# Performance work log

Measured on AMD Instinct MI355X. Metric: run time of the kernel, lower is better.

## Reference

```python
import jax, jax.numpy as jnp
import numpy as np

NEG_SLOPE = 0.2

def leaky_relu(x):
    return jnp.where(x >= 0, x, NEG_SLOPE * x)

def conv1x1(x, w, b):
    # x: [n,c,h,w], w: [o,c], b: [o]
    return jnp.einsum('nchw,oc->nohw', x, w) + b[None, :, None, None]

def setup_inputs() -> dict:
    key = jax.random.key(0)
    ks = jax.random.split(key, 7)
    n, c, h, w = 4, 64, 80, 80
    scale = 1.0 / np.sqrt(c)
    return {
        'x': jax.random.normal(ks[0], (n, c, h, w), dtype=jnp.float32),
        'w1': jax.random.normal(ks[1], (c, c), dtype=jnp.float32) * scale,
        'b1': jax.random.normal(ks[2], (c,), dtype=jnp.float32) * 0.01,
        'w2': jax.random.normal(ks[3], (c, c), dtype=jnp.float32) * scale,
        'b2': jax.random.normal(ks[4], (c,), dtype=jnp.float32) * 0.01,
        'w3': jax.random.normal(ks[5], (c, c), dtype=jnp.float32) * scale,
        'b3': jax.random.normal(ks[6], (c,), dtype=jnp.float32) * 0.01,
    }

def reference(x, w1, b1, w2, b2, w3, b3):
    n, c, h, w = x.shape
    e1 = leaky_relu(conv1x1(x, w1, b1))  # [n,c,h,w]
    e2 = leaky_relu(conv1x1(x, w2, b2))
    asm = leaky_relu(conv1x1(x, w3, b3))
    # q: [n, hw, c]; k: [n, c, hw]
    q = e1.transpose(0, 2, 3, 1).reshape(n, h * w, c)
    k = e2.reshape(n, c, h * w)
    score = jax.nn.softmax(jnp.matmul(q, k), axis=2)  # [n, hw, hw]
    v = asm.reshape(n, c, h * w).transpose(0, 2, 1)   # [n, hw, c]
    out = jnp.matmul(score, v)                        # [n, hw, c]
    return out.transpose(0, 2, 1).reshape(n, c, h, w)
```

## Files before the change

### kernel.cpp

```cpp
#include <hip/hip_runtime.h>


typedef __attribute__((ext_vector_type(8))) unsigned short us8;
typedef __attribute__((ext_vector_type(4))) unsigned short us4;
typedef __attribute__((ext_vector_type(8))) __bf16 bf16x8;
typedef __attribute__((ext_vector_type(16))) float f32x16;

#define HW 6400
#define L2E 1.44269504088896340736f
#define SHIFT 32.0f
#define KS 10
#define ITERS 10

union V8 { us8 s; us4 h[2]; bf16x8 b; unsigned u4[4]; };

__device__ __forceinline__ unsigned short f32_to_bf16(float f) {
  unsigned u = __float_as_uint(f);
  u += 0x7fffu + ((u >> 16) & 1u);
  return (unsigned short)(u >> 16);
}
__device__ __forceinline__ float bf16_bits_to_f32(unsigned short u) {
  return __uint_as_float(((unsigned)u) << 16);
}
__device__ __forceinline__ unsigned pack_bf16x2(float a, float b) {
#if __has_builtin(__builtin_amdgcn_cvt_pk_bf16_f32)
  auto v = __builtin_amdgcn_cvt_pk_bf16_f32(a, b);
  unsigned u;
  __builtin_memcpy(&u, &v, 4);
  return u;
#else
  unsigned ua = __float_as_uint(a); ua += 0x7fffu + ((ua >> 16) & 1u);
  unsigned ub = __float_as_uint(b); ub += 0x7fffu + ((ub >> 16) & 1u);
  return (ua >> 16) | (ub & 0xffff0000u);
#endif
}

__device__ __forceinline__ void split_hilo(const float* f, V8& hi, V8& lo) {
#pragma unroll
  for (int j = 0; j < 8; ++j) {
    const unsigned short h = f32_to_bf16(f[j]);
    const float r = f[j] - bf16_bits_to_f32(h);
    hi.s[j] = h;
    lo.s[j] = f32_to_bf16(r);
  }
}

__global__ __launch_bounds__(256, 2) void conv_kernel(
    const float* __restrict__ x,
    const float* __restrict__ w1, const float* __restrict__ b1,
    const float* __restrict__ w2, const float* __restrict__ b2,
    const float* __restrict__ w3, const float* __restrict__ b3,
    unsigned short* __restrict__ Qg, unsigned short* __restrict__ Kg,
    unsigned short* __restrict__ Vg) {
  __shared__ __align__(16) float xs[64 * 132];
  __shared__ __align__(16) unsigned short tb[128 * 72];

  const int t = threadIdx.x;
  const int n = blockIdx.y;
  const int p0 = blockIdx.x * 128;
  const int wv = t >> 6;
  const int lane = t & 63;
  const int l31 = lane & 31;
  const int lh = lane >> 5;
  const int ob = (wv & 1) * 32;
  const int pw = (wv >> 1) * 64;

  {
    const int c = t >> 2, qq = t & 3;
    const float* src = x + ((size_t)(n * 64 + c) * HW + p0 + qq * 32);
    float* dst = xs + c * 132 + qq * 32;
#pragma unroll
    for (int i = 0; i < 8; ++i)
      *(float4*)(dst + i * 4) = *(const float4*)(src + i * 4);
  }
  __syncthreads();

  const float* wms[3] = {w1, w2, w3};
  const float* bms[3] = {b1, b2, b3};

#pragma unroll 1
  for (int k = 0; k < 3; ++k) {
    const float* wm = wms[k];
    const float* bm = bms[k];

    V8 ah[4], al[4];
#pragma unroll
    for (int kst = 0; kst < 4; ++kst) {
      const float* wr = wm + (size_t)(ob + l31) * 64 + kst * 16 + lh * 8;
      float wf[8];
      *(float4*)(wf) = *(const float4*)wr;
      *(float4*)(wf + 4) = *(const float4*)(wr + 4);
      split_hilo(wf, ah[kst], al[kst]);
    }

    f32x16 acc[2];
#pragma unroll
    for (int pb = 0; pb < 2; ++pb)
#pragma unroll
      for (int r = 0; r < 16; ++r) acc[pb][r] = 0.f;

#pragma unroll
    for (int kst = 0; kst < 4; ++kst) {
#pragma unroll
      for (int pb = 0; pb < 2; ++pb) {
        float xf[8];
        const float* xp = xs + (kst * 16 + lh * 8) * 132 + pw + pb * 32 + l31;
#pragma unroll
        for (int j = 0; j < 8; ++j) xf[j] = xp[j * 132];
        V8 bh, bl;
        split_hilo(xf, bh, bl);
        acc[pb] = __builtin_amdgcn_mfma_f32_32x32x16_bf16(al[kst].b, bh.b, acc[pb], 0, 0, 0);
        acc[pb] = __builtin_amdgcn_mfma_f32_32x32x16_bf16(ah[kst].b, bl.b, acc[pb], 0, 0, 0);
        acc[pb] = __builtin_amdgcn_mfma_f32_32x32x16_bf16(ah[kst].b, bh.b, acc[pb], 0, 0, 0);
      }
    }

    if (k < 2) {
#pragma unroll
      for (int pb = 0; pb < 2; ++pb) {
#pragma unroll
        for (int rq = 0; rq < 4; ++rq) {
          const int o = ob + 8 * rq + 4 * lh;
          const int pcol = pw + pb * 32 + l31;
          float v[4];
#pragma unroll
          for (int j = 0; j < 4; ++j) {
            float a = acc[pb][4 * rq + j] + bm[o + j];
            a = fmaxf(a, 0.f) + 0.2f * fminf(a, 0.f);
            if (k == 0) a *= L2E;
            v[j] = a;
          }
          unsigned* dst = (unsigned*)(tb + pcol * 72 + o);
          dst[0] = pack_bf16x2(v[0], v[1]);
          dst[1] = pack_bf16x2(v[2], v[3]);
        }
      }
      __syncthreads();
      {
        const int p = t >> 1, half = t & 1;
        const unsigned short* src = tb + p * 72 + half * 32;
        unsigned short* dst = (k == 0 ? Qg : Kg) +
                              (size_t)(n * HW + p0 + p) * 64 + half * 32;
#pragma unroll
        for (int i = 0; i < 4; ++i) *(us8*)(dst + i * 8) = *(const us8*)(src + i * 8);
      }
      __syncthreads();
    } else {
#pragma unroll
      for (int pb = 0; pb < 2; ++pb) {
#pragma unroll
        for (int r = 0; r < 16; ++r) {
          const int o = ob + 8 * (r >> 2) + 4 * lh + (r & 3);
          const int pcol = pw + pb * 32 + l31;
          float a = acc[pb][r] + bm[o];
          a = fmaxf(a, 0.f) + 0.2f * fminf(a, 0.f);
          Vg[(size_t)(n * 64 + o) * HW + p0 + pcol] = f32_to_bf16(a);
        }
      }
    }
  }
}

__global__ __launch_bounds__(256, 2) void attn_kernel(
    const unsigned short* __restrict__ Qg, const unsigned short* __restrict__ Kg,
    const unsigned short* __restrict__ Vg, unsigned short* __restrict__ Opart,
    float* __restrict__ Lpart) {
  __shared__ __align__(16) char smem[36864];
  unsigned short* Otb = (unsigned short*)smem;

  const int t = threadIdx.x;
  const int w = t >> 6;
  const int lane = t & 63;
  const int l31 = lane & 31;
  const int lh = lane >> 5;
  const int nb = blockIdx.y;
  const int qb = blockIdx.x * 256;
  const int ks = blockIdx.z;
  const int key0 = ks * (HW / KS);

  V8 aQ[2][4];
#pragma unroll
  for (int qh = 0; qh < 2; ++qh) {
    const unsigned short* qrow =
        Qg + (size_t)(nb * HW + qb + w * 64 + qh * 32 + l31) * 64 + lh * 8;
#pragma unroll
    for (int kst = 0; kst < 4; ++kst) aQ[qh][kst].s = *(const us8*)(qrow + kst * 16);
  }

  f32x16 accO[2][2];
#pragma unroll
  for (int qh = 0; qh < 2; ++qh)
#pragma unroll
    for (int ci = 0; ci < 2; ++ci)
#pragma unroll
      for (int r = 0; r < 16; ++r) accO[qh][ci][r] = 0.f;
  float lp[2] = {0.f, 0.f};

  const int soff = (t >> 2) * 72 + (t & 3) * 16;
  const unsigned short* ksrc =
      Kg + (size_t)nb * HW * 64 + (size_t)(key0 + (t >> 2)) * 64 + (t & 3) * 16;
  const unsigned short* vsrc =
      Vg + (size_t)nb * 64 * HW + (size_t)(t >> 2) * HW + key0 + (t & 3) * 16;

  V8 kr0, kr1, vr0, vr1;
  kr0.s = *(const us8*)ksrc;
  kr1.s = *(const us8*)(ksrc + 8);
  vr0.s = *(const us8*)vsrc;
  vr1.s = *(const us8*)(vsrc + 8);
  {
    unsigned short* kd = (unsigned short*)smem + soff;
    unsigned short* vd = (unsigned short*)(smem + 18432) + soff;
    *(us8*)kd = kr0.s; *(us8*)(kd + 8) = kr1.s;
    *(us8*)vd = vr0.s; *(us8*)(vd + 8) = vr1.s;
  }
  __syncthreads();

#pragma unroll 1
  for (int jt = 0; jt < ITERS; ++jt) {
    const int b = jt & 1;
    const unsigned short* Kc = (const unsigned short*)(smem + b * 9216);
    const unsigned short* Vc = (const unsigned short*)(smem + 18432 + b * 9216);
    const bool more = (jt + 1 < ITERS);

    if (more) {
      kr0.s = *(const us8*)(ksrc + (jt + 1) * 4096);
      kr1.s = *(const us8*)(ksrc + (jt + 1) * 4096 + 8);
      vr0.s = *(const us8*)(vsrc + (jt + 1) * 64);
      vr1.s = *(const us8*)(vsrc + (jt + 1) * 64 + 8);
    }

    V8 ak[2][4];
#pragma unroll
    for (int ni = 0; ni < 2; ++ni)
#pragma unroll
      for (int kst = 0; kst < 4; ++kst)
        ak[ni][kst].s = *(const us8*)(Kc + (ni * 32 + l31) * 72 + kst * 16 + lh * 8);

    uint2 pkq[2][2][4];
#pragma unroll
    for (int qh = 0; qh < 2; ++qh) {
#pragma unroll
      for (int ni = 0; ni < 2; ++ni) {
        f32x16 sacc;
#pragma unroll
        for (int r = 0; r < 16; ++r) sacc[r] = -SHIFT;
#pragma unroll
        for (int kst = 0; kst < 4; ++kst)
          sacc = __builtin_amdgcn_mfma_f32_32x32x16_bf16(ak[ni][kst].b,
                                                         aQ[qh][kst].b, sacc, 0, 0, 0);
#pragma unroll
        for (int g = 0; g < 4; ++g) {
          const float p0 = __builtin_amdgcn_exp2f(sacc[4 * g + 0]);
          const float p1 = __builtin_amdgcn_exp2f(sacc[4 * g + 1]);
          const float p2 = __builtin_amdgcn_exp2f(sacc[4 * g + 2]);
          const float p3 = __builtin_amdgcn_exp2f(sacc[4 * g + 3]);
          lp[qh] += (p0 + p1) + (p2 + p3);
          pkq[qh][ni][g].x = pack_bf16x2(p0, p1);
          pkq[qh][ni][g].y = pack_bf16x2(p2, p3);
        }
      }
    }

    V8 bv[2][4];
#pragma unroll
    for (int ci = 0; ci < 2; ++ci)
#pragma unroll
      for (int kst = 0; kst < 4; ++kst)
        bv[ci][kst].s = *(const us8*)(Vc + (ci * 32 + l31) * 72 + kst * 16 + lh * 8);

#pragma unroll
    for (int qh = 0; qh < 2; ++qh) {
#pragma unroll
      for (int kst = 0; kst < 4; ++kst) {
        const int ni = kst >> 1;
        const int gb = 2 * (kst & 1);
        const uint2 qa = pkq[qh][ni][gb];
        const uint2 qb2 = pkq[qh][ni][gb + 1];
        uint2 send;
        send.x = lh ? qa.x : qb2.x;
        send.y = lh ? qa.y : qb2.y;
        uint2 recv;
        recv.x = __shfl_xor(send.x, 32);
        recv.y = __shfl_xor(send.y, 32);
        const uint2 keep = {lh ? qb2.x : qa.x, lh ? qb2.y : qa.y};
        V8 ap;
        ap.u4[0] = lh ? recv.x : keep.x;
        ap.u4[1] = lh ? recv.y : keep.y;
        ap.u4[2] = lh ? keep.x : recv.x;
        ap.u4[3] = lh ? keep.y : recv.y;
        accO[qh][0] = __builtin_amdgcn_mfma_f32_32x32x16_bf16(ap.b, bv[0][kst].b,
                                                              accO[qh][0], 0, 0, 0);
        accO[qh][1] = __builtin_amdgcn_mfma_f32_32x32x16_bf16(ap.b, bv[1][kst].b,
                                                              accO[qh][1], 0, 0, 0);
      }
    }

    if (more) {
      unsigned short* kd = (unsigned short*)(smem + (1 - b) * 9216) + soff;
      unsigned short* vd = (unsigned short*)(smem + 18432 + (1 - b) * 9216) + soff;
      *(us8*)kd = kr0.s; *(us8*)(kd + 8) = kr1.s;
      *(us8*)vd = vr0.s; *(us8*)(vd + 8) = vr1.s;
      __syncthreads();
    }
  }

#pragma unroll
  for (int qh = 0; qh < 2; ++qh) {
    const float lsum = lp[qh] + __shfl_xor(lp[qh], 32);
    if (lh == 0)
      Lpart[((size_t)ks * 4 + nb) * HW + qb + w * 64 + qh * 32 + l31] = lsum;
  }

#pragma unroll 1
  for (int pi = 0; pi < 2; ++pi) {
    __syncthreads();
    if ((w >> 1) == pi) {
#pragma unroll
      for (int qh = 0; qh < 2; ++qh)
#pragma unroll
        for (int ci = 0; ci < 2; ++ci)
#pragma unroll
          for (int r = 0; r < 16; ++r) {
            const int qcol = (w & 1) * 64 + qh * 32 + 8 * (r >> 2) + 4 * lh + (r & 3);
            Otb[(ci * 32 + l31) * 132 + qcol] = f32_to_bf16(accO[qh][ci][r]);
          }
    }
    __syncthreads();
    {
      const int ch = t >> 2, part = t & 3;
      const unsigned short* src = Otb + ch * 132 + part * 32;
      unsigned short* dst = Opart + (((size_t)ks * 4 + nb) * 64 + ch) * HW +
                            qb + pi * 128 + part * 32;
#pragma unroll
      for (int i = 0; i < 4; ++i) {
        V8 v;
        v.h[0] = *(const us4*)(src + i * 8);
        v.h[1] = *(const us4*)(src + i * 8 + 4);
        *(us8*)(dst + i * 8) = v.s;
      }
    }
  }
}

__global__ __launch_bounds__(256) void combine_kernel(
    const unsigned short* __restrict__ Opart, const float* __restrict__ Lpart,
    float* __restrict__ out) {
  const int tid = blockIdx.x * 256 + threadIdx.x;
  const size_t e = (size_t)tid * 4;
  float4 o = {0.f, 0.f, 0.f, 0.f};
#pragma unroll
  for (int ks = 0; ks < KS; ++ks) {
    const us4 v = *(const us4*)(Opart + (size_t)ks * (4 * 64 * HW) + e);
    o.x += bf16_bits_to_f32(v[0]);
    o.y += bf16_bits_to_f32(v[1]);
    o.z += bf16_bits_to_f32(v[2]);
    o.w += bf16_bits_to_f32(v[3]);
  }
  const int n = (int)(e / (64 * HW));
  const int p = (int)(e % HW);
  float4 l = {0.f, 0.f, 0.f, 0.f};
#pragma unroll
  for (int ks = 0; ks < KS; ++ks) {
    const float4 v = *(const float4*)(Lpart + ((size_t)ks * 4 + n) * HW + p);
    l.x += v.x; l.y += v.y; l.z += v.z; l.w += v.w;
  }
  float4 r;
  r.x = o.x / l.x; r.y = o.y / l.y; r.z = o.z / l.z; r.w = o.w / l.w;
  *(float4*)(out + e) = r;
}

extern "C" void kernel_launch(void* const* d_in, const int* in_sizes, int n_in,
                              void* d_out, int out_size, void* d_ws, size_t ws_size,
                              hipStream_t stream) {
  const float* x = (const float*)d_in[0];
  const float* w1 = (const float*)d_in[1];
  const float* b1 = (const float*)d_in[2];
  const float* w2 = (const float*)d_in[3];
  const float* b2 = (const float*)d_in[4];
  const float* w3 = (const float*)d_in[5];
  const float* b3 = (const float*)d_in[6];
  float* out = (float*)d_out;

  unsigned short* Q = (unsigned short*)d_ws;
  unsigned short* K = Q + (size_t)4 * HW * 64;
  unsigned short* V = K + (size_t)4 * HW * 64;
  unsigned short* Opart = V + (size_t)4 * HW * 64;
  float* Lpart = (float*)(Opart + (size_t)KS * 4 * 64 * HW);

  conv_kernel<<<dim3(50, 4), 256, 0, stream>>>(x, w1, b1, w2, b2, w3, b3,
                                               Q, K, V);
  attn_kernel<<<dim3(25, 4, KS), 256, 0, stream>>>(Q, K, V, Opart, Lpart);
  combine_kernel<<<1600, 256, 0, stream>>>(Opart, Lpart, out);
}
```

Baseline: 155.5 us.

## Load attention K/V fragments directly from global memory, drop LDS staging

The attention kernel stops staging K and V tiles through double-buffered shared memory with per-iteration barriers. Each wave now reads its MFMA operand fragments straight from global memory (relying on L1/L2 for reuse across the four waves). The loop is reorganized per key-half so S, softmax exp and PV run in smaller chunks with fewer live registers. Occupancy hint rises to 3 blocks per CU, and the grid is flattened to a 1D launch with a remapped block index that places blocks sharing the same batch and key split close together for cache locality. Risks are redundant global/L2 traffic (each wave fetches the same K/V) and exposed load latency without software prefetch.

```diff
diff --git a/kernel.cpp b/kernel.cpp
--- a/kernel.cpp
+++ b/kernel.cpp
@@ -161,21 +161,24 @@
   }
 }
 
-__global__ __launch_bounds__(256, 2) void attn_kernel(
+__global__ __launch_bounds__(256, 3) void attn_kernel(
     const unsigned short* __restrict__ Qg, const unsigned short* __restrict__ Kg,
     const unsigned short* __restrict__ Vg, unsigned short* __restrict__ Opart,
     float* __restrict__ Lpart) {
-  __shared__ __align__(16) char smem[36864];
-  unsigned short* Otb = (unsigned short*)smem;
+  __shared__ __align__(16) unsigned short Otb[64 * 132];
 
   const int t = threadIdx.x;
   const int w = t >> 6;
   const int lane = t & 63;
   const int l31 = lane & 31;
   const int lh = lane >> 5;
-  const int nb = blockIdx.y;
-  const int qb = blockIdx.x * 256;
-  const int ks = blockIdx.z;
+
+  const int id = blockIdx.x;
+  const int nb = (id >> 1) & 3;
+  const int j = ((id >> 3) << 1) | (id & 1);
+  const int qi = j % 25;
+  const int ks = j / 25;
+  const int qb = qi * 256;
   const int key0 = ks * (HW / KS);
 
   V8 aQ[2][4];
@@ -196,58 +199,40 @@
       for (int r = 0; r < 16; ++r) accO[qh][ci][r] = 0.f;
   float lp[2] = {0.f, 0.f};
 
-  const int soff = (t >> 2) * 72 + (t & 3) * 16;
-  const unsigned short* ksrc =
-      Kg + (size_t)nb * HW * 64 + (size_t)(key0 + (t >> 2)) * 64 + (t & 3) * 16;
-  const unsigned short* vsrc =
-      Vg + (size_t)nb * 64 * HW + (size_t)(t >> 2) * HW + key0 + (t & 3) * 16;
-
-  V8 kr0, kr1, vr0, vr1;
-  kr0.s = *(const us8*)ksrc;
-  kr1.s = *(const us8*)(ksrc + 8);
-  vr0.s = *(const us8*)vsrc;
-  vr1.s = *(const us8*)(vsrc + 8);
-  {
-    unsigned short* kd = (unsigned short*)smem + soff;
-    unsigned short* vd = (unsigned short*)(smem + 18432) + soff;
-    *(us8*)kd = kr0.s; *(us8*)(kd + 8) = kr1.s;
-    *(us8*)vd = vr0.s; *(us8*)(vd + 8) = vr1.s;
-  }
-  __syncthreads();
+  const unsigned short* kfrag =
+      Kg + (size_t)(nb * HW + key0 + l31) * 64 + lh * 8;
+  const unsigned short* vfrag =
+      Vg + (size_t)nb * 64 * HW + (size_t)l31 * HW + key0 + lh * 8;
 
 #pragma unroll 1
   for (int jt = 0; jt < ITERS; ++jt) {
-    const int b = jt & 1;
-    const unsigned short* Kc = (const unsigned short*)(smem + b * 9216);
-    const unsigned short* Vc = (const unsigned short*)(smem + 18432 + b * 9216);
-    const bool more = (jt + 1 < ITERS);
-
-    if (more) {
-      kr0.s = *(const us8*)(ksrc + (jt + 1) * 4096);
-      kr1.s = *(const us8*)(ksrc + (jt + 1) * 4096 + 8);
-      vr0.s = *(const us8*)(vsrc + (jt + 1) * 64);
-      vr1.s = *(const us8*)(vsrc + (jt + 1) * 64 + 8);
-    }
-
-    V8 ak[2][4];
-#pragma unroll
-    for (int ni = 0; ni < 2; ++ni)
+    const unsigned short* kit = kfrag + jt * 4096;
+    const unsigned short* vit = vfrag + jt * 64;
+
+#pragma unroll
+    for (int ni = 0; ni < 2; ++ni) {
+      V8 ak[4];
 #pragma unroll
       for (int kst = 0; kst < 4; ++kst)
-        ak[ni][kst].s = *(const us8*)(Kc + (ni * 32 + l31) * 72 + kst * 16 + lh * 8);
-
-    uint2 pkq[2][2][4];
-#pragma unroll
-    for (int qh = 0; qh < 2; ++qh) {
-#pragma unroll
-      for (int ni = 0; ni < 2; ++ni) {
+        ak[kst].s = *(const us8*)(kit + ni * 2048 + kst * 16);
+      V8 bv[2][2];
+#pragma unroll
+      for (int ci = 0; ci < 2; ++ci)
+#pragma unroll
+        for (int kk = 0; kk < 2; ++kk)
+          bv[ci][kk].s =
+              *(const us8*)(vit + (size_t)ci * 32 * HW + (2 * ni + kk) * 16);
+
+#pragma unroll
+      for (int qh = 0; qh < 2; ++qh) {
         f32x16 sacc;
 #pragma unroll
         for (int r = 0; r < 16; ++r) sacc[r] = -SHIFT;
 #pragma unroll
         for (int kst = 0; kst < 4; ++kst)
-          sacc = __builtin_amdgcn_mfma_f32_32x32x16_bf16(ak[ni][kst].b,
+          sacc = __builtin_amdgcn_mfma_f32_32x32x16_bf16(ak[kst].b,
                                                          aQ[qh][kst].b, sacc, 0, 0, 0);
+        uint2 pkg[4];
 #pragma unroll
         for (int g = 0; g < 4; ++g) {
           const float p0 = __builtin_amdgcn_exp2f(sacc[4 * g + 0]);
@@ -255,52 +240,32 @@
           const float p2 = __builtin_amdgcn_exp2f(sacc[4 * g + 2]);
           const float p3 = __builtin_amdgcn_exp2f(sacc[4 * g + 3]);
           lp[qh] += (p0 + p1) + (p2 + p3);
-          pkq[qh][ni][g].x = pack_bf16x2(p0, p1);
-          pkq[qh][ni][g].y = pack_bf16x2(p2, p3);
+          pkg[g].x = pack_bf16x2(p0, p1);
+          pkg[g].y = pack_bf16x2(p2, p3);
         }
-      }
-    }
-
-    V8 bv[2][4];
-#pragma unroll
-    for (int ci = 0; ci < 2; ++ci)
-#pragma unroll
-      for (int kst = 0; kst < 4; ++kst)
-        bv[ci][kst].s = *(const us8*)(Vc + (ci * 32 + l31) * 72 + kst * 16 + lh * 8);
-
-#pragma unroll
-    for (int qh = 0; qh < 2; ++qh) {
-#pragma unroll
-      for (int kst = 0; kst < 4; ++kst) {
-        const int ni = kst >> 1;
-        const int gb = 2 * (kst & 1);
-        const uint2 qa = pkq[qh][ni][gb];
-        const uint2 qb2 = pkq[qh][ni][gb + 1];
-        uint2 send;
-        send.x = lh ? qa.x : qb2.x;
-        send.y = lh ? qa.y : qb2.y;
-        uint2 recv;
-        recv.x = __shfl_xor(send.x, 32);
-        recv.y = __shfl_xor(send.y, 32);
-        const uint2 keep = {lh ? qb2.x : qa.x, lh ? qb2.y : qa.y};
-        V8 ap;
-        ap.u4[0] = lh ? recv.x : keep.x;
-        ap.u4[1] = lh ? recv.y : keep.y;
-        ap.u4[2] = lh ? keep.x : recv.x;
-        ap.u4[3] = lh ? keep.y : recv.y;
-        accO[qh][0] = __builtin_amdgcn_mfma_f32_32x32x16_bf16(ap.b, bv[0][kst].b,
-                                                              accO[qh][0], 0, 0, 0);
-        accO[qh][1] = __builtin_amdgcn_mfma_f32_32x32x16_bf16(ap.b, bv[1][kst].b,
-                                                              accO[qh][1], 0, 0, 0);
-      }
-    }
-
-    if (more) {
-      unsigned short* kd = (unsigned short*)(smem + (1 - b) * 9216) + soff;
-      unsigned short* vd = (unsigned short*)(smem + 18432 + (1 - b) * 9216) + soff;
-      *(us8*)kd = kr0.s; *(us8*)(kd + 8) = kr1.s;
-      *(us8*)vd = vr0.s; *(us8*)(vd + 8) = vr1.s;
-      __syncthreads();
+#pragma unroll
+        for (int kk = 0; kk < 2; ++kk) {
+          const int gb = 2 * kk;
+          const uint2 qa = pkg[gb];
+          const uint2 qb2 = pkg[gb + 1];
+          uint2 send;
+          send.x = lh ? qa.x : qb2.x;
+          send.y = lh ? qa.y : qb2.y;
+          uint2 recv;
+          recv.x = __shfl_xor(send.x, 32);
+          recv.y = __shfl_xor(send.y, 32);
+          const uint2 keep = {lh ? qb2.x : qa.x, lh ? qb2.y : qa.y};
+          V8 ap;
+          ap.u4[0] = lh ? recv.x : keep.x;
+          ap.u4[1] = lh ? recv.y : keep.y;
+          ap.u4[2] = lh ? keep.x : recv.x;
+          ap.u4[3] = lh ? keep.y : recv.y;
+          accO[qh][0] = __builtin_amdgcn_mfma_f32_32x32x16_bf16(
+              ap.b, bv[0][kk].b, accO[qh][0], 0, 0, 0);
+          accO[qh][1] = __builtin_amdgcn_mfma_f32_32x32x16_bf16(
+              ap.b, bv[1][kk].b, accO[qh][1], 0, 0, 0);
+        }
+      }
     }
   }
 
@@ -389,6 +354,6 @@
 
   conv_kernel<<<dim3(50, 4), 256, 0, stream>>>(x, w1, b1, w2, b2, w3, b3,
                                                Q, K, V);
-  attn_kernel<<<dim3(25, 4, KS), 256, 0, stream>>>(Q, K, V, Opart, Lpart);
+  attn_kernel<<<1000, 256, 0, stream>>>(Q, K, V, Opart, Lpart);
   combine_kernel<<<1600, 256, 0, stream>>>(Opart, Lpart, out);
 }
```

Result: slower. 346.0 us (+122.6%).

## Shrink per-wave query tile and halve key splits to raise attention occupancy

Applied to the files above, without the earlier changes.

Each wave now handles 32 queries instead of 64, so a block covers 128 queries. The split-K factor drops from 10 to 5, with twice as many key iterations per block, and launch bounds allow 4 blocks per CU. The smaller register footprint is meant to raise occupancy, and fewer key splits reduce the partial-output traffic written and then read by the combine kernel. In exchange, each K/V tile in shared memory is reused across fewer queries, which doubles LDS reads per flop. The constant score shift of -32 is removed, which relies on the scores staying within exp2 range.

```diff
diff --git a/kernel.cpp b/kernel.cpp
--- a/kernel.cpp
+++ b/kernel.cpp
@@ -8,9 +8,8 @@
 
 #define HW 6400
 #define L2E 1.44269504088896340736f
-#define SHIFT 32.0f
-#define KS 10
-#define ITERS 10
+#define KS 5
+#define ITERS 20
 
 union V8 { us8 s; us4 h[2]; bf16x8 b; unsigned u4[4]; };
 
@@ -161,7 +160,7 @@
   }
 }
 
-__global__ __launch_bounds__(256, 2) void attn_kernel(
+__global__ __launch_bounds__(256, 4) void attn_kernel(
     const unsigned short* __restrict__ Qg, const unsigned short* __restrict__ Kg,
     const unsigned short* __restrict__ Vg, unsigned short* __restrict__ Opart,
     float* __restrict__ Lpart) {
@@ -174,27 +173,24 @@
   const int l31 = lane & 31;
   const int lh = lane >> 5;
   const int nb = blockIdx.y;
-  const int qb = blockIdx.x * 256;
+  const int qb = blockIdx.x * 128;
   const int ks = blockIdx.z;
   const int key0 = ks * (HW / KS);
 
-  V8 aQ[2][4];
-#pragma unroll
-  for (int qh = 0; qh < 2; ++qh) {
+  V8 aQ[4];
+  {
     const unsigned short* qrow =
-        Qg + (size_t)(nb * HW + qb + w * 64 + qh * 32 + l31) * 64 + lh * 8;
-#pragma unroll
-    for (int kst = 0; kst < 4; ++kst) aQ[qh][kst].s = *(const us8*)(qrow + kst * 16);
-  }
-
-  f32x16 accO[2][2];
-#pragma unroll
-  for (int qh = 0; qh < 2; ++qh)
-#pragma unroll
-    for (int ci = 0; ci < 2; ++ci)
-#pragma unroll
-      for (int r = 0; r < 16; ++r) accO[qh][ci][r] = 0.f;
-  float lp[2] = {0.f, 0.f};
+        Qg + (size_t)(nb * HW + qb + w * 32 + l31) * 64 + lh * 8;
+#pragma unroll
+    for (int kst = 0; kst < 4; ++kst) aQ[kst].s = *(const us8*)(qrow + kst * 16);
+  }
+
+  f32x16 accO[2];
+#pragma unroll
+  for (int ci = 0; ci < 2; ++ci)
+#pragma unroll
+    for (int r = 0; r < 16; ++r) accO[ci][r] = 0.f;
+  float lp = 0.f;
 
   const int soff = (t >> 2) * 72 + (t & 3) * 16;
   const unsigned short* ksrc =
@@ -229,53 +225,43 @@
       vr1.s = *(const us8*)(vsrc + (jt + 1) * 64 + 8);
     }
 
-    V8 ak[2][4];
-#pragma unroll
-    for (int ni = 0; ni < 2; ++ni)
+#pragma unroll
+    for (int ni = 0; ni < 2; ++ni) {
+      V8 ak[4];
 #pragma unroll
       for (int kst = 0; kst < 4; ++kst)
-        ak[ni][kst].s = *(const us8*)(Kc + (ni * 32 + l31) * 72 + kst * 16 + lh * 8);
-
-    uint2 pkq[2][2][4];
-#pragma unroll
-    for (int qh = 0; qh < 2; ++qh) {
-#pragma unroll
-      for (int ni = 0; ni < 2; ++ni) {
-        f32x16 sacc;
-#pragma unroll
-        for (int r = 0; r < 16; ++r) sacc[r] = -SHIFT;
-#pragma unroll
-        for (int kst = 0; kst < 4; ++kst)
-          sacc = __builtin_amdgcn_mfma_f32_32x32x16_bf16(ak[ni][kst].b,
-                                                         aQ[qh][kst].b, sacc, 0, 0, 0);
-#pragma unroll
-        for (int g = 0; g < 4; ++g) {
-          const float p0 = __builtin_amdgcn_exp2f(sacc[4 * g + 0]);
-          const float p1 = __builtin_amdgcn_exp2f(sacc[4 * g + 1]);
-          const float p2 = __builtin_amdgcn_exp2f(sacc[4 * g + 2]);
-          const float p3 = __builtin_amdgcn_exp2f(sacc[4 * g + 3]);
-          lp[qh] += (p0 + p1) + (p2 + p3);
-          pkq[qh][ni][g].x = pack_bf16x2(p0, p1);
-          pkq[qh][ni][g].y = pack_bf16x2(p2, p3);
-        }
-      }
-    }
-
-    V8 bv[2][4];
-#pragma unroll
-    for (int ci = 0; ci < 2; ++ci)
+        ak[kst].s = *(const us8*)(Kc + (ni * 32 + l31) * 72 + kst * 16 + lh * 8);
+      f32x16 sacc;
+#pragma unroll
+      for (int r = 0; r < 16; ++r) sacc[r] = 0.f;
 #pragma unroll
       for (int kst = 0; kst < 4; ++kst)
-        bv[ci][kst].s = *(const us8*)(Vc + (ci * 32 + l31) * 72 + kst * 16 + lh * 8);
-
-#pragma unroll
-    for (int qh = 0; qh < 2; ++qh) {
-#pragma unroll
-      for (int kst = 0; kst < 4; ++kst) {
-        const int ni = kst >> 1;
-        const int gb = 2 * (kst & 1);
-        const uint2 qa = pkq[qh][ni][gb];
-        const uint2 qb2 = pkq[qh][ni][gb + 1];
+        sacc = __builtin_amdgcn_mfma_f32_32x32x16_bf16(ak[kst].b, aQ[kst].b,
+                                                       sacc, 0, 0, 0);
+      uint2 pkg[4];
+#pragma unroll
+      for (int g = 0; g < 4; ++g) {
+        const float p0 = __builtin_amdgcn_exp2f(sacc[4 * g + 0]);
+        const float p1 = __builtin_amdgcn_exp2f(sacc[4 * g + 1]);
+        const float p2 = __builtin_amdgcn_exp2f(sacc[4 * g + 2]);
+        const float p3 = __builtin_amdgcn_exp2f(sacc[4 * g + 3]);
+        lp += (p0 + p1) + (p2 + p3);
+        pkg[g].x = pack_bf16x2(p0, p1);
+        pkg[g].y = pack_bf16x2(p2, p3);
+      }
+
+      V8 bv[2][2];
+#pragma unroll
+      for (int ci = 0; ci < 2; ++ci)
+#pragma unroll
+        for (int kk = 0; kk < 2; ++kk)
+          bv[ci][kk].s = *(const us8*)(Vc + (ci * 32 + l31) * 72 +
+                                       (2 * ni + kk) * 16 + lh * 8);
+#pragma unroll
+      for (int kk = 0; kk < 2; ++kk) {
+        const int gb = 2 * kk;
+        const uint2 qa = pkg[gb];
+        const uint2 qb2 = pkg[gb + 1];
         uint2 send;
         send.x = lh ? qa.x : qb2.x;
         send.y = lh ? qa.y : qb2.y;
@@ -288,10 +274,10 @@
         ap.u4[1] = lh ? recv.y : keep.y;
         ap.u4[2] = lh ? keep.x : recv.x;
         ap.u4[3] = lh ? keep.y : recv.y;
-        accO[qh][0] = __builtin_amdgcn_mfma_f32_32x32x16_bf16(ap.b, bv[0][kst].b,
-                                                              accO[qh][0], 0, 0, 0);
-        accO[qh][1] = __builtin_amdgcn_mfma_f32_32x32x16_bf16(ap.b, bv[1][kst].b,
-                                                              accO[qh][1], 0, 0, 0);
+        accO[0] = __builtin_amdgcn_mfma_f32_32x32x16_bf16(ap.b, bv[0][kk].b,
+                                                          accO[0], 0, 0, 0);
+        accO[1] = __builtin_amdgcn_mfma_f32_32x32x16_bf16(ap.b, bv[1][kk].b,
+                                                          accO[1], 0, 0, 0);
       }
     }
 
@@ -304,40 +290,32 @@
     }
   }
 
-#pragma unroll
-  for (int qh = 0; qh < 2; ++qh) {
-    const float lsum = lp[qh] + __shfl_xor(lp[qh], 32);
+  {
+    const float lsum = lp + __shfl_xor(lp, 32);
     if (lh == 0)
-      Lpart[((size_t)ks * 4 + nb) * HW + qb + w * 64 + qh * 32 + l31] = lsum;
-  }
-
-#pragma unroll 1
-  for (int pi = 0; pi < 2; ++pi) {
-    __syncthreads();
-    if ((w >> 1) == pi) {
-#pragma unroll
-      for (int qh = 0; qh < 2; ++qh)
-#pragma unroll
-        for (int ci = 0; ci < 2; ++ci)
-#pragma unroll
-          for (int r = 0; r < 16; ++r) {
-            const int qcol = (w & 1) * 64 + qh * 32 + 8 * (r >> 2) + 4 * lh + (r & 3);
-            Otb[(ci * 32 + l31) * 132 + qcol] = f32_to_bf16(accO[qh][ci][r]);
-          }
-    }
-    __syncthreads();
-    {
-      const int ch = t >> 2, part = t & 3;
-      const unsigned short* src = Otb + ch * 132 + part * 32;
-      unsigned short* dst = Opart + (((size_t)ks * 4 + nb) * 64 + ch) * HW +
-                            qb + pi * 128 + part * 32;
-#pragma unroll
-      for (int i = 0; i < 4; ++i) {
-        V8 v;
-        v.h[0] = *(const us4*)(src + i * 8);
-        v.h[1] = *(const us4*)(src + i * 8 + 4);
-        *(us8*)(dst + i * 8) = v.s;
-      }
+      Lpart[((size_t)ks * 4 + nb) * HW + qb + w * 32 + l31] = lsum;
+  }
+
+  __syncthreads();
+#pragma unroll
+  for (int ci = 0; ci < 2; ++ci)
+#pragma unroll
+    for (int r = 0; r < 16; ++r) {
+      const int qcol = w * 32 + 8 * (r >> 2) + 4 * lh + (r & 3);
+      Otb[(ci * 32 + l31) * 132 + qcol] = f32_to_bf16(accO[ci][r]);
+    }
+  __syncthreads();
+  {
+    const int ch = t >> 2, part = t & 3;
+    const unsigned short* src = Otb + ch * 132 + part * 32;
+    unsigned short* dst =
+        Opart + (((size_t)ks * 4 + nb) * 64 + ch) * HW + qb + part * 32;
+#pragma unroll
+    for (int i = 0; i < 4; ++i) {
+      V8 v;
+      v.h[0] = *(const us4*)(src + i * 8);
+      v.h[1] = *(const us4*)(src + i * 8 + 4);
+      *(us8*)(dst + i * 8) = v.s;
     }
   }
 }
@@ -389,6 +367,6 @@
 
   conv_kernel<<<dim3(50, 4), 256, 0, stream>>>(x, w1, b1, w2, b2, w3, b3,
                                                Q, K, V);
-  attn_kernel<<<dim3(25, 4, KS), 256, 0, stream>>>(Q, K, V, Opart, Lpart);
+  attn_kernel<<<dim3(50, 4, KS), 256, 0, stream>>>(Q, K, V, Opart, Lpart);
   combine_kernel<<<1600, 256, 0, stream>>>(Opart, Lpart, out);
 }
```

Result: faster. 150.7 us (-3.1%).
